# Optimization experiments

Measured on AMD Instinct MI355X. Metric: run time of the kernel, lower is better.

The kernel has to match this reference:

```python
import jax, jax.numpy as jnp
import numpy as np

EPS = 1e-8
EPS12 = 1e-12
TAU = 0.2
IOU_THRESHOLD = 0.5
NEG_INF = -1e9

N, C = 8192, 1024
HID, FGD, CLSD = 256, 64, 128


def setup_inputs() -> dict:
    key = jax.random.key(0)
    ks = jax.random.split(key, 16)
    roi_feats = jax.random.normal(ks[0], (N, C), dtype=jnp.float32)
    # labels in {-1 (ignore), 0 (bg), 1..20 (classes)}
    labels = jax.random.randint(ks[1], (N,), 0, 21, dtype=jnp.int64) - 1
    ious = jax.random.uniform(ks[2], (N,), dtype=jnp.float32)
    s = 0.02
    w1f = jax.random.normal(ks[3], (HID, C), dtype=jnp.float32) * s
    b1f = jnp.zeros((HID,), dtype=jnp.float32)
    w2f = jax.random.normal(ks[4], (FGD, HID), dtype=jnp.float32) * s
    b2f = jnp.zeros((FGD,), dtype=jnp.float32)
    w1c = jax.random.normal(ks[5], (HID, C), dtype=jnp.float32) * s
    b1c = jnp.zeros((HID,), dtype=jnp.float32)
    w2c = jax.random.normal(ks[6], (CLSD, HID), dtype=jnp.float32) * s
    b2c = jnp.zeros((CLSD,), dtype=jnp.float32)
    return {"roi_feats": roi_feats, "labels": labels, "ious": ious,
            "w1f": w1f, "b1f": b1f, "w2f": w2f, "b2f": b2f,
            "w1c": w1c, "b1c": b1c, "w2c": w2c, "b2c": b2c}


def _project_normalize(x, w1, b1, w2, b2):
    h = jax.nn.relu(x @ w1.T + b1)
    z = h @ w2.T + b2
    nrm = jnp.linalg.norm(z, axis=1, keepdims=True)  # F.normalize: z / max(||z||, eps)
    return z / jnp.maximum(nrm, EPS)


def _fg_bg_loss(z_fg, fg_mask, ignore_mask, iou_weight):
    n = z_fg.shape[0]
    anchor = fg_mask & ~ignore_mask
    eye = jnp.eye(n, dtype=bool)
    # pos_mask[i,j] = fg_mask[j] & ~ignore[j], self excluded
    pos = (fg_mask & ~ignore_mask)[None, :] & ~eye  # [N,N]
    sim = (z_fg @ z_fg.T) / TAU
    sim_exp = jnp.exp(sim) * (~eye).astype(sim.dtype)
    denom = sim_exp.sum(axis=1)  # [N]
    numer = jnp.sum(jnp.exp(sim) * pos.astype(sim.dtype), axis=1)  # [N]
    n_pos = pos.sum(axis=1)
    loss_i = -jnp.log((numer + EPS) / (denom + EPS))
    valid = anchor & (n_pos > 0)
    w = iou_weight
    num = jnp.sum(jnp.where(valid, loss_i * w, 0.0))
    den = jnp.sum(jnp.where(valid, w, 0.0)) + EPS
    return num / den


def _class_supcon_loss(z_cls, labels, fg_mask, ignore_mask, iou_weight):
    n = z_cls.shape[0]
    anchor = fg_mask & ~ignore_mask
    eye = jnp.eye(n, dtype=bool)
    valid_den = ~eye & ~ignore_mask[None, :]  # [N,N]
    # pos[i,j]: same label, j not ignored, labels[j] != 0, j != i, j valid
    pos = (labels[None, :] == labels[:, None]) & ~ignore_mask[None, :] & (labels[None, :] != 0)
    pos = pos & ~eye & valid_den
    sim = (z_cls @ z_cls.T) / TAU
    logits = jnp.where(valid_den, sim, NEG_INF)
    denom_log = jax.nn.logsumexp(logits, axis=1)  # [N]
    n_pos = pos.sum(axis=1)
    sum_pos = jnp.sum(jnp.where(pos, sim, 0.0), axis=1)
    n_pos_safe = jnp.maximum(n_pos, 1).astype(sim.dtype)
    loss_i = -(sum_pos - n_pos.astype(sim.dtype) * denom_log) / n_pos_safe
    valid = anchor & (n_pos > 0) & valid_den.any(axis=1)
    w = iou_weight
    num = jnp.sum(jnp.where(valid, loss_i * w, 0.0))
    den = jnp.sum(jnp.where(valid, w, 0.0)) + EPS12
    return num / den


def reference(roi_feats, labels, ious, w1f, b1f, w2f, b2f, w1c, b1c, w2c, b2c):
    z_fg = _project_normalize(roi_feats, w1f, b1f, w2f, b2f)
    z_cls = _project_normalize(roi_feats, w1c, b1c, w2c, b2c)
    ignore_mask = labels == -1
    bg_mask = (labels == 0) & ~ignore_mask
    fg_mask = (labels > 0) & ~ignore_mask
    iou_weight = jnp.where(ious > IOU_THRESHOLD, ious, 0.0)
    loss_fg_bg = _fg_bg_loss(z_fg, fg_mask, ignore_mask, iou_weight)
    loss_supcon = _class_supcon_loss(z_cls, labels, fg_mask, ignore_mask, iou_weight)
    # loss_weights = (1.0, 1.0); stacked as [loss_fg_bg, loss_supcon]
    return jnp.stack([loss_fg_bg * 1.0, loss_supcon * 1.0])
```

## Files before the change

### kernel.cpp

```cpp
#include <hip/hip_runtime.h>
#include <hip/hip_bf16.h>
#include <math.h>

#define N_ROI 8192
#define C_IN  1024
#define HIDD  256
#define FGD   64
#define CLSD  128
#define INV_TAU 5.0f
#define SCALE_LOG2E 7.2134752f
#define LN2F 0.69314718f

using frag_ab = __attribute__((ext_vector_type(8))) short;
using f32x16  = __attribute__((ext_vector_type(16))) float;

static __device__ __forceinline__ short f32_to_bf16_bits(float f) {
  unsigned u = __builtin_bit_cast(unsigned, f);
  u = (u + 0x7FFFu + ((u >> 16) & 1u)) >> 16;
  return (short)u;
}
static __device__ __forceinline__ float bf16_bits_to_f32(short b) {
  unsigned u = ((unsigned)(unsigned short)b) << 16;
  return __builtin_bit_cast(float, u);
}
static __device__ __forceinline__ float fast_exp2(float x) {
#if __has_builtin(__builtin_amdgcn_exp2f)
  return __builtin_amdgcn_exp2f(x);
#else
  return exp2f(x);
#endif
}

__global__ void prep_zero_kernel(float* accum, int* cnt) {
  int t = threadIdx.x;
  if (t < 8) accum[t] = 0.f;
  if (t < 24) cnt[t] = 0;
}

__global__ void prep_stats_kernel(const int* __restrict__ labels,
                                  float* __restrict__ Sfg, float* __restrict__ Pfg,
                                  float* __restrict__ Scls, float* __restrict__ SPc,
                                  float* __restrict__ pfv, float* __restrict__ nimv,
                                  float* __restrict__ ljmv, int* __restrict__ cnt) {
  int i = blockIdx.x * blockDim.x + threadIdx.x;
  if (i >= N_ROI) return;
  Sfg[i] = 0.f; Pfg[i] = 0.f; Scls[i] = 0.f; SPc[i] = 0.f;
  int l = labels[i];
  pfv[i]  = (l > 0)  ? 1.f : 0.f;
  nimv[i] = (l != -1) ? 1.f : 0.f;
  ljmv[i] = (l > 0)  ? (float)l : -7.f;
  int b = l + 1; if (b < 0) b = 0; if (b > 21) b = 21;
  atomicAdd(&cnt[b], 1);
}

__global__ __launch_bounds__(256) void pack_w_kernel(
    const float* __restrict__ w1f, const float* __restrict__ w1c,
    const float* __restrict__ w2f, const float* __restrict__ w2c,
    short* __restrict__ W1pf, short* __restrict__ W1pc,
    short* __restrict__ W2pf, short* __restrict__ W2pc) {
  int b = blockIdx.x;
  const float* src; short* dst; int Ksh; int b0;
  if (b < 128)      { src = w1f; dst = W1pf; Ksh = 10; b0 = 0; }
  else if (b < 256) { src = w1c; dst = W1pc; Ksh = 10; b0 = 128; }
  else if (b < 264) { src = w2f; dst = W2pf; Ksh = 8;  b0 = 256; }
  else              { src = w2c; dst = W2pc; Ksh = 8;  b0 = 264; }
  int K = 1 << Ksh;
  int f = (b - b0) * 256 + threadIdx.x;
  int r = f >> (Ksh - 3);
  int c0 = (f & ((K >> 3) - 1)) << 3;
  float4 v0 = *(const float4*)(src + (size_t)r * K + c0);
  float4 v1 = *(const float4*)(src + (size_t)r * K + c0 + 4);
  union { short s[8]; uint4 v; } o;
  o.s[0] = f32_to_bf16_bits(v0.x); o.s[1] = f32_to_bf16_bits(v0.y);
  o.s[2] = f32_to_bf16_bits(v0.z); o.s[3] = f32_to_bf16_bits(v0.w);
  o.s[4] = f32_to_bf16_bits(v1.x); o.s[5] = f32_to_bf16_bits(v1.y);
  o.s[6] = f32_to_bf16_bits(v1.z); o.s[7] = f32_to_bf16_bits(v1.w);
  ((uint4*)dst)[(size_t)((r >> 5) * (K >> 4) + (c0 >> 4)) * 64 +
                ((c0 >> 3) & 1) * 32 + (r & 31)] = o.v;
}

__global__ __launch_bounds__(256) void gemm1_kernel(
    const float* __restrict__ X,
    const short* __restrict__ W1pf, const short* __restrict__ W1pc,
    const float* __restrict__ b1f, const float* __restrict__ b1c,
    short* __restrict__ Hpf, short* __restrict__ Hpc) {
  __shared__ union {
    short stageA[2][1024];
    short T[4][128 * 36];
  } sm;
  int tid = threadIdx.x, lane = tid & 63, wv = tid >> 6;
  int Mb = blockIdx.x;
  const short* Wp = (wv >> 1) ? W1pc : W1pf;
  const float* b1 = (wv >> 1) ? b1c  : b1f;
  short*       Hp = (wv >> 1) ? Hpc  : Hpf;
  const uint4* Wv4 = (const uint4*)Wp;
  int arow = tid >> 3;
  int ac4  = tid & 7;
  const float* Xp = X + (size_t)(Mb * 32 + arow) * C_IN + ac4 * 4;
  int aslot = ((ac4 >> 2) * 64 + ((ac4 >> 1) & 1) * 32 + arow) * 8 + (ac4 & 1) * 4;

  float4 av;
  frag_ab breg[2][8];
  f32x16 acc[4];
  #pragma unroll
  for (int nt = 0; nt < 4; ++nt)
    #pragma unroll
    for (int q = 0; q < 16; ++q) acc[nt][q] = 0.f;

  auto loadA = [&](int c) { av = *(const float4*)(Xp + c * 32); };
  auto loadB = [&](int c, int s) {
    #pragma unroll
    for (int kci = 0; kci < 2; ++kci)
      #pragma unroll
      for (int nt = 0; nt < 4; ++nt)
        breg[s][kci * 4 + nt] =
            *(const frag_ab*)&Wv4[(size_t)(((wv & 1) * 4 + nt) * 64 + c * 2 + kci) * 64 + lane];
  };
  auto storeA = [&](int buf) {
    *(short4*)&sm.stageA[buf][aslot] =
        make_short4(f32_to_bf16_bits(av.x), f32_to_bf16_bits(av.y),
                    f32_to_bf16_bits(av.z), f32_to_bf16_bits(av.w));
  };
  auto domfma = [&](int buf, int bank) {
    frag_ab a0 = *(const frag_ab*)&sm.stageA[buf][(0 * 64 + lane) * 8];
    frag_ab a1 = *(const frag_ab*)&sm.stageA[buf][(1 * 64 + lane) * 8];
    #pragma unroll
    for (int nt = 0; nt < 4; ++nt)
      acc[nt] = __builtin_amdgcn_mfma_f32_32x32x16_bf16(a0, breg[bank][nt], acc[nt], 0, 0, 0);
    #pragma unroll
    for (int nt = 0; nt < 4; ++nt)
      acc[nt] = __builtin_amdgcn_mfma_f32_32x32x16_bf16(a1, breg[bank][4 + nt], acc[nt], 0, 0, 0);
  };

  loadA(0); loadB(0, 0); storeA(0);
  __syncthreads();
  for (int c = 0; c < 32; c += 2) {
    if (c + 1 < 32) { loadA(c + 1); loadB(c + 1, 1); }
    domfma(0, 0);
    if (c + 1 < 32) storeA(1);
    __syncthreads();
    if (c + 2 < 32) { loadA(c + 2); loadB(c + 2, 0); }
    domfma(1, 1);
    if (c + 2 < 32) storeA(0);
    __syncthreads();
  }
  int cl31 = lane & 31, h = lane >> 5;
  short* T = sm.T[wv];
  #pragma unroll
  for (int nt = 0; nt < 4; ++nt) {
    int colLocal = nt * 32 + cl31;
    float bb = b1[(wv & 1) * 128 + colLocal];
    #pragma unroll
    for (int g = 0; g < 4; ++g) {
      float x0 = fmaxf(acc[nt][g * 4 + 0] + bb, 0.f);
      float x1 = fmaxf(acc[nt][g * 4 + 1] + bb, 0.f);
      float x2 = fmaxf(acc[nt][g * 4 + 2] + bb, 0.f);
      float x3 = fmaxf(acc[nt][g * 4 + 3] + bb, 0.f);
      *(short4*)&T[colLocal * 36 + 4 * h + 8 * g] =
          make_short4(f32_to_bf16_bits(x0), f32_to_bf16_bits(x1),
                      f32_to_bf16_bits(x2), f32_to_bf16_bits(x3));
    }
  }
  __syncthreads();
  uint4* Hv4 = (uint4*)Hp;
  #pragma unroll
  for (int k = 0; k < 8; ++k) {
    union { short s[8]; uint4 v; } o;
    int c0 = k * 16 + h * 8;
    #pragma unroll
    for (int e = 0; e < 8; ++e) o.s[e] = T[(c0 + e) * 36 + cl31];
    Hv4[(size_t)(Mb * 16 + (wv & 1) * 8 + k) * 64 + h * 32 + cl31] = o.v;
  }
}

template<int D>
__device__ __forceinline__ void gemm2_head(
    const short* __restrict__ Hp, const short* __restrict__ W2p,
    const float* __restrict__ b2, short* __restrict__ Zr,
    float* __restrict__ tii, short* __restrict__ T, int gt) {
  int lane = threadIdx.x & 63;
  const frag_ab* Hv = (const frag_ab*)Hp;
  const frag_ab* Wv = (const frag_ab*)W2p;
  constexpr int NT = D / 32;
  frag_ab a[16];
  #pragma unroll
  for (int kc = 0; kc < 16; ++kc) a[kc] = Hv[(size_t)(gt * 16 + kc) * 64 + lane];
  f32x16 acc[NT];
  #pragma unroll
  for (int j = 0; j < NT; ++j)
    #pragma unroll
    for (int q = 0; q < 16; ++q) acc[j][q] = 0.f;
  #pragma unroll
  for (int kc = 0; kc < 16; ++kc)
    #pragma unroll
    for (int j = 0; j < NT; ++j)
      acc[j] = __builtin_amdgcn_mfma_f32_32x32x16_bf16(a[kc], Wv[(j * 16 + kc) * 64 + lane], acc[j], 0, 0, 0);
  int c = lane & 31, h = lane >> 5;
  float bb[NT];
  #pragma unroll
  for (int j = 0; j < NT; ++j) bb[j] = b2[j * 32 + c];
  float s1[16];
  #pragma unroll
  for (int r = 0; r < 16; ++r) {
    s1[r] = 0.f;
    #pragma unroll
    for (int j = 0; j < NT; ++j) {
      float v = acc[j][r] + bb[j];
      s1[r] += v * v;
    }
  }
  #pragma unroll
  for (int r = 0; r < 16; ++r)
    #pragma unroll
    for (int m = 1; m < 32; m <<= 1) s1[r] += __shfl_xor(s1[r], m);
  float s2[16];
  #pragma unroll
  for (int r = 0; r < 16; ++r) s2[r] = 0.f;
  #pragma unroll
  for (int j = 0; j < NT; ++j) {
    int cl = j * 32 + c;
    #pragma unroll
    for (int g = 0; g < 4; ++g) {
      short q0, q1, q2, q3;
      #pragma unroll
      for (int e = 0; e < 4; ++e) {
        int r = g * 4 + e;
        float sc = 1.f / fmaxf(sqrtf(s1[r]), 1e-8f);
        short qb = f32_to_bf16_bits((acc[j][r] + bb[j]) * sc);
        float zf = bf16_bits_to_f32(qb);
        s2[r] += zf * zf;
        if (e == 0) q0 = qb; else if (e == 1) q1 = qb; else if (e == 2) q2 = qb; else q3 = qb;
      }
      *(short4*)&T[cl * 36 + 4 * h + 8 * g] = make_short4(q0, q1, q2, q3);
    }
  }
  #pragma unroll
  for (int r = 0; r < 16; ++r)
    #pragma unroll
    for (int m = 1; m < 32; m <<= 1) s2[r] += __shfl_xor(s2[r], m);
  if (c == 0) {
    #pragma unroll
    for (int r = 0; r < 16; ++r)
      tii[gt * 32 + (r & 3) + 8 * (r >> 2) + 4 * h] = s2[r];
  }
  __syncthreads();
  uint4* Zv = (uint4*)Zr;
  #pragma unroll
  for (int k = 0; k < D / 16; ++k) {
    int c0 = (2 * k + h) * 8;
    union { short s[8]; uint4 u; } o;
    #pragma unroll
    for (int e = 0; e < 8; ++e) o.s[e] = T[(c0 + e) * 36 + c];
    Zv[(size_t)(gt * (D / 16) + k) * 64 + h * 32 + c] = o.u;
  }
}

__global__ __launch_bounds__(128) void gemm2_kernel(
    const short* __restrict__ Hpf, const short* __restrict__ Hpc,
    const short* __restrict__ W2pf, const short* __restrict__ W2pc,
    const float* __restrict__ b2f, const float* __restrict__ b2c,
    short* __restrict__ Zrf, short* __restrict__ Zrc,
    float* __restrict__ tiif, float* __restrict__ tiic) {
  __shared__ short T2[2][128 * 36];
  int wv = threadIdx.x >> 6;
  int b = blockIdx.x;
  if (b < 128)
    gemm2_head<64>(Hpf, W2pf, b2f, Zrf, tiif, T2[wv], b * 2 + wv);
  else
    gemm2_head<128>(Hpc, W2pc, b2c, Zrc, tiic, T2[wv], (b - 128) * 2 + wv);
}

template<int D, int MODE, int NJT>
__device__ __forceinline__ void loss_body(
    const short* __restrict__ Zr, const int* __restrict__ labels,
    const float* __restrict__ pfv, const float* __restrict__ nimv,
    const float* __restrict__ ljmv,
    float* __restrict__ Sg, float* __restrict__ Pg) {
  constexpr int KC = D / 16;
  int tid = threadIdx.x, lane = tid & 63, wv = tid >> 6;
  int itile = blockIdx.x * 4 + wv;
  const frag_ab* Zrv = (const frag_ab*)Zr;
  frag_ab a[KC];
  #pragma unroll
  for (int kc = 0; kc < KC; ++kc) {
    frag_ab t = Zrv[(itile * KC + kc) * 64 + lane];
    #pragma unroll
    for (int e = 0; e < 8; ++e)
      t[e] = f32_to_bf16_bits(bf16_bits_to_f32(t[e]) * SCALE_LOG2E);
    a[kc] = t;
  }
  float limf[16];
  if (MODE == 1) {
    #pragma unroll
    for (int r = 0; r < 16; ++r) {
      int row = (r & 3) + 8 * (r >> 2) + 4 * (lane >> 5);
      limf[r] = (float)labels[itile * 32 + row];
    }
  }
  float Ssum[16] = {}, Psum[16] = {};
  int jt0 = blockIdx.y * NJT;
  int jlane = lane & 31;

  #pragma unroll 2
  for (int kk = 0; kk < NJT; ++kk) {
    int jt = jt0 + kk;
    int j = jt * 32 + jlane;
    float pf = 0.f, nim = 0.f, ljm = 0.f;
    if (MODE == 0) pf = pfv[j];
    else { nim = nimv[j]; ljm = ljmv[j]; }
    f32x16 acc;
    #pragma unroll
    for (int q = 0; q < 16; ++q) acc[q] = 0.f;
    #pragma unroll
    for (int kc = 0; kc < KC; ++kc) {
      frag_ab b = Zrv[((size_t)jt * KC + kc) * 64 + lane];
      acc = __builtin_amdgcn_mfma_f32_32x32x16_bf16(a[kc], b, acc, 0, 0, 0);
    }
    #pragma unroll
    for (int rr = 0; rr < 16; ++rr) {
      float e = fast_exp2(acc[rr]);
      if (MODE == 0) {
        Ssum[rr] += e;
        Psum[rr] = fmaf(pf, e, Psum[rr]);
      } else {
        Ssum[rr] = fmaf(nim, e, Ssum[rr]);
        Psum[rr] += (limf[rr] == ljm) ? acc[rr] : 0.f;
      }
    }
  }
  #pragma unroll
  for (int r = 0; r < 16; ++r) {
    float s = Ssum[r], p = Psum[r];
    #pragma unroll
    for (int m = 1; m < 32; m <<= 1) { s += __shfl_xor(s, m); p += __shfl_xor(p, m); }
    if ((lane & 31) == 0) {
      if (MODE == 1) p *= LN2F;
      int row = (r & 3) + 8 * (r >> 2) + 4 * (lane >> 5);
      atomicAdd(&Sg[itile * 32 + row], s);
      atomicAdd(&Pg[itile * 32 + row], p);
    }
  }
}

__global__ __launch_bounds__(256, 4) void loss_kernel(
    const short* __restrict__ Zrf, const short* __restrict__ Zrc,
    const int* __restrict__ labels,
    const float* __restrict__ pfv, const float* __restrict__ nimv,
    const float* __restrict__ ljmv,
    float* __restrict__ Sfg, float* __restrict__ Pfg,
    float* __restrict__ Scls, float* __restrict__ SPc) {
  if (blockIdx.z == 0)
    loss_body<FGD, 0, 16>(Zrf, labels, pfv, nimv, ljmv, Sfg, Pfg);
  else
    loss_body<CLSD, 1, 16>(Zrc, labels, pfv, nimv, ljmv, Scls, SPc);
}

__global__ __launch_bounds__(256) void finalize_kernel(
    const float* __restrict__ Sfg, const float* __restrict__ Pfg,
    const float* __restrict__ Scls, const float* __restrict__ SPc,
    const float* __restrict__ tiif, const float* __restrict__ tiic,
    const int* __restrict__ labels, const float* __restrict__ ious,
    int* __restrict__ cnt, float* __restrict__ accum, float* __restrict__ out) {
  int i = blockIdx.x * 256 + threadIdx.x;
  int l = labels[i];
  float iv = ious[i];
  float w = (iv > 0.5f) ? iv : 0.f;
  int cntP = 0;
  #pragma unroll
  for (int b = 2; b <= 21; ++b) cntP += cnt[b];
  int cntNI = N_ROI - cnt[0];
  bool Pi = (l > 0);
  float numF = 0.f, denF = 0.f, numC = 0.f, denC = 0.f;
  float eF = __expf(INV_TAU * tiif[i]);
  float Sf = Sfg[i] - eF;
  float Pf = Pfg[i] - (Pi ? eF : 0.f);
  int nposF = cntP - (Pi ? 1 : 0);
  if (Pi && nposF > 0) {
    float lossF = logf((Sf + 1e-8f) / (Pf + 1e-8f));
    numF = lossF * w; denF = w;
  }
  float tC = INV_TAU * tiic[i];
  float eC = __expf(tC);
  float Sc = Scls[i] - ((l != -1) ? eC : 0.f);
  float SP = SPc[i] - (Pi ? tC : 0.f);
  int nposC = Pi ? (cnt[l + 1] - 1) : 0;
  bool anyv = (cntNI - ((l != -1) ? 1 : 0)) > 0;
  if (Pi && nposC > 0 && anyv) {
    float lse = logf(Sc);
    float lossC = -(SP - (float)nposC * lse) / fmaxf((float)nposC, 1.f);
    numC = lossC * w; denC = w;
  }
  float v0 = numF, v1 = denF, v2 = numC, v3 = denC;
  #pragma unroll
  for (int m = 1; m < 64; m <<= 1) {
    v0 += __shfl_xor(v0, m); v1 += __shfl_xor(v1, m);
    v2 += __shfl_xor(v2, m); v3 += __shfl_xor(v3, m);
  }
  __shared__ float red[4][4];
  int lane = threadIdx.x & 63, wid = threadIdx.x >> 6;
  if (lane == 0) { red[wid][0]=v0; red[wid][1]=v1; red[wid][2]=v2; red[wid][3]=v3; }
  __syncthreads();
  if (threadIdx.x == 0) {
    float s0=0,s1=0,s2=0,s3=0;
    for (int q = 0; q < 4; ++q) { s0+=red[q][0]; s1+=red[q][1]; s2+=red[q][2]; s3+=red[q][3]; }
    atomicAdd(&accum[0], s0); atomicAdd(&accum[1], s1);
    atomicAdd(&accum[2], s2); atomicAdd(&accum[3], s3);
    __threadfence();
    int t = atomicAdd(&cnt[22], 1);
    if (t == 31) {
      __threadfence();
      out[0] = accum[0] / (accum[1] + 1e-8f);
      out[1] = accum[2] / (accum[3] + 1e-12f);
    }
  }
}

extern "C" void kernel_launch(void* const* d_in, const int* in_sizes, int n_in,
                              void* d_out, int out_size, void* d_ws, size_t ws_size,
                              hipStream_t stream) {
  const float* X    = (const float*)d_in[0];
  const int*  labels= (const int*)d_in[1];
  const float* ious = (const float*)d_in[2];
  const float* w1f  = (const float*)d_in[3];
  const float* b1f  = (const float*)d_in[4];
  const float* w2f  = (const float*)d_in[5];
  const float* b2f  = (const float*)d_in[6];
  const float* w1c  = (const float*)d_in[7];
  const float* b1c  = (const float*)d_in[8];
  const float* w2c  = (const float*)d_in[9];
  const float* b2c  = (const float*)d_in[10];
  float* out = (float*)d_out;

  char* w = (char*)d_ws;
  short* W1pf = (short*)w;            w += 524288;
  short* W1pc = (short*)w;            w += 524288;
  short* W2pf = (short*)w;            w += 32768;
  short* W2pc = (short*)w;            w += 65536;
  short* Hpf  = (short*)w;            w += 4194304;
  short* Hpc  = (short*)w;            w += 4194304;
  short* Zrf  = (short*)w;            w += 1048576;
  short* Zrc  = (short*)w;            w += 2097152;
  float* Sfg  = (float*)w;            w += 32768;
  float* Pfg  = (float*)w;            w += 32768;
  float* Scls = (float*)w;            w += 32768;
  float* SPc  = (float*)w;            w += 32768;
  float* tiif = (float*)w;            w += 32768;
  float* tiic = (float*)w;            w += 32768;
  float* pfv  = (float*)w;            w += 32768;
  float* nimv = (float*)w;            w += 32768;
  float* ljmv = (float*)w;            w += 32768;
  float* accum= (float*)w;            w += 32;
  int*   cnt  = (int*)w;              w += 96;

  prep_zero_kernel<<<1, 64, 0, stream>>>(accum, cnt);
  prep_stats_kernel<<<N_ROI/256, 256, 0, stream>>>(labels, Sfg, Pfg, Scls, SPc,
                                                   pfv, nimv, ljmv, cnt);
  pack_w_kernel<<<280, 256, 0, stream>>>(w1f, w1c, w2f, w2c, W1pf, W1pc, W2pf, W2pc);

  gemm1_kernel<<<256, 256, 0, stream>>>(X, W1pf, W1pc, b1f, b1c, Hpf, Hpc);
  gemm2_kernel<<<256, 128, 0, stream>>>(Hpf, Hpc, W2pf, W2pc, b2f, b2c,
                                        Zrf, Zrc, tiif, tiic);

  loss_kernel<<<dim3(64, 16, 2), 256, 0, stream>>>(Zrf, Zrc, labels, pfv, nimv, ljmv,
                                                   Sfg, Pfg, Scls, SPc);

  finalize_kernel<<<N_ROI/256, 256, 0, stream>>>(Sfg, Pfg, Scls, SPc, tiif, tiic,
                                                 labels, ious, cnt, accum, out);
}
```

Baseline: 214.7 us.

## Fuse gemm1, gemm2 and label stats into one MLP kernel via LDS

Merges the first projection GEMM, the second GEMM with normalization, and the per-ROI label statistics into a single kernel. The hidden activations stay in shared memory instead of making a round trip through global memory. The accumulator zeroing moves into an extra block of the weight-packing kernel, cutting the launch count from five to two. In exchange, only two of the four waves run the second GEMM while the other two sit idle, and the kernel's larger LDS footprint may lower occupancy.

Measured after the change: 204.9 us. -4.6%, faster.

```diff
diff --git a/kernel.cpp b/kernel.cpp
--- a/kernel.cpp
+++ b/kernel.cpp
@@ -31,34 +31,19 @@
 #endif
 }
 
-__global__ void prep_zero_kernel(float* accum, int* cnt) {
-  int t = threadIdx.x;
-  if (t < 8) accum[t] = 0.f;
-  if (t < 24) cnt[t] = 0;
-}
-
-__global__ void prep_stats_kernel(const int* __restrict__ labels,
-                                  float* __restrict__ Sfg, float* __restrict__ Pfg,
-                                  float* __restrict__ Scls, float* __restrict__ SPc,
-                                  float* __restrict__ pfv, float* __restrict__ nimv,
-                                  float* __restrict__ ljmv, int* __restrict__ cnt) {
-  int i = blockIdx.x * blockDim.x + threadIdx.x;
-  if (i >= N_ROI) return;
-  Sfg[i] = 0.f; Pfg[i] = 0.f; Scls[i] = 0.f; SPc[i] = 0.f;
-  int l = labels[i];
-  pfv[i]  = (l > 0)  ? 1.f : 0.f;
-  nimv[i] = (l != -1) ? 1.f : 0.f;
-  ljmv[i] = (l > 0)  ? (float)l : -7.f;
-  int b = l + 1; if (b < 0) b = 0; if (b > 21) b = 21;
-  atomicAdd(&cnt[b], 1);
-}
-
-__global__ __launch_bounds__(256) void pack_w_kernel(
+__global__ __launch_bounds__(256) void pack_zero_kernel(
     const float* __restrict__ w1f, const float* __restrict__ w1c,
     const float* __restrict__ w2f, const float* __restrict__ w2c,
     short* __restrict__ W1pf, short* __restrict__ W1pc,
-    short* __restrict__ W2pf, short* __restrict__ W2pc) {
+    short* __restrict__ W2pf, short* __restrict__ W2pc,
+    float* __restrict__ accum, int* __restrict__ cnt) {
   int b = blockIdx.x;
+  if (b == 280) {
+    int t = threadIdx.x;
+    if (t < 8) accum[t] = 0.f;
+    if (t < 24) cnt[t] = 0;
+    return;
+  }
   const float* src; short* dst; int Ksh; int b0;
   if (b < 128)      { src = w1f; dst = W1pf; Ksh = 10; b0 = 0; }
   else if (b < 256) { src = w1c; dst = W1pc; Ksh = 10; b0 = 128; }
@@ -79,112 +64,19 @@
                 ((c0 >> 3) & 1) * 32 + (r & 31)] = o.v;
 }
 
-__global__ __launch_bounds__(256) void gemm1_kernel(
-    const float* __restrict__ X,
-    const short* __restrict__ W1pf, const short* __restrict__ W1pc,
-    const float* __restrict__ b1f, const float* __restrict__ b1c,
-    short* __restrict__ Hpf, short* __restrict__ Hpc) {
-  __shared__ union {
-    short stageA[2][1024];
-    short T[4][128 * 36];
-  } sm;
-  int tid = threadIdx.x, lane = tid & 63, wv = tid >> 6;
-  int Mb = blockIdx.x;
-  const short* Wp = (wv >> 1) ? W1pc : W1pf;
-  const float* b1 = (wv >> 1) ? b1c  : b1f;
-  short*       Hp = (wv >> 1) ? Hpc  : Hpf;
-  const uint4* Wv4 = (const uint4*)Wp;
-  int arow = tid >> 3;
-  int ac4  = tid & 7;
-  const float* Xp = X + (size_t)(Mb * 32 + arow) * C_IN + ac4 * 4;
-  int aslot = ((ac4 >> 2) * 64 + ((ac4 >> 1) & 1) * 32 + arow) * 8 + (ac4 & 1) * 4;
-
-  float4 av;
-  frag_ab breg[2][8];
-  f32x16 acc[4];
-  #pragma unroll
-  for (int nt = 0; nt < 4; ++nt)
-    #pragma unroll
-    for (int q = 0; q < 16; ++q) acc[nt][q] = 0.f;
-
-  auto loadA = [&](int c) { av = *(const float4*)(Xp + c * 32); };
-  auto loadB = [&](int c, int s) {
-    #pragma unroll
-    for (int kci = 0; kci < 2; ++kci)
-      #pragma unroll
-      for (int nt = 0; nt < 4; ++nt)
-        breg[s][kci * 4 + nt] =
-            *(const frag_ab*)&Wv4[(size_t)(((wv & 1) * 4 + nt) * 64 + c * 2 + kci) * 64 + lane];
-  };
-  auto storeA = [&](int buf) {
-    *(short4*)&sm.stageA[buf][aslot] =
-        make_short4(f32_to_bf16_bits(av.x), f32_to_bf16_bits(av.y),
-                    f32_to_bf16_bits(av.z), f32_to_bf16_bits(av.w));
-  };
-  auto domfma = [&](int buf, int bank) {
-    frag_ab a0 = *(const frag_ab*)&sm.stageA[buf][(0 * 64 + lane) * 8];
-    frag_ab a1 = *(const frag_ab*)&sm.stageA[buf][(1 * 64 + lane) * 8];
-    #pragma unroll
-    for (int nt = 0; nt < 4; ++nt)
-      acc[nt] = __builtin_amdgcn_mfma_f32_32x32x16_bf16(a0, breg[bank][nt], acc[nt], 0, 0, 0);
-    #pragma unroll
-    for (int nt = 0; nt < 4; ++nt)
-      acc[nt] = __builtin_amdgcn_mfma_f32_32x32x16_bf16(a1, breg[bank][4 + nt], acc[nt], 0, 0, 0);
-  };
-
-  loadA(0); loadB(0, 0); storeA(0);
-  __syncthreads();
-  for (int c = 0; c < 32; c += 2) {
-    if (c + 1 < 32) { loadA(c + 1); loadB(c + 1, 1); }
-    domfma(0, 0);
-    if (c + 1 < 32) storeA(1);
-    __syncthreads();
-    if (c + 2 < 32) { loadA(c + 2); loadB(c + 2, 0); }
-    domfma(1, 1);
-    if (c + 2 < 32) storeA(0);
-    __syncthreads();
-  }
-  int cl31 = lane & 31, h = lane >> 5;
-  short* T = sm.T[wv];
-  #pragma unroll
-  for (int nt = 0; nt < 4; ++nt) {
-    int colLocal = nt * 32 + cl31;
-    float bb = b1[(wv & 1) * 128 + colLocal];
-    #pragma unroll
-    for (int g = 0; g < 4; ++g) {
-      float x0 = fmaxf(acc[nt][g * 4 + 0] + bb, 0.f);
-      float x1 = fmaxf(acc[nt][g * 4 + 1] + bb, 0.f);
-      float x2 = fmaxf(acc[nt][g * 4 + 2] + bb, 0.f);
-      float x3 = fmaxf(acc[nt][g * 4 + 3] + bb, 0.f);
-      *(short4*)&T[colLocal * 36 + 4 * h + 8 * g] =
-          make_short4(f32_to_bf16_bits(x0), f32_to_bf16_bits(x1),
-                      f32_to_bf16_bits(x2), f32_to_bf16_bits(x3));
-    }
-  }
-  __syncthreads();
-  uint4* Hv4 = (uint4*)Hp;
-  #pragma unroll
-  for (int k = 0; k < 8; ++k) {
-    union { short s[8]; uint4 v; } o;
-    int c0 = k * 16 + h * 8;
-    #pragma unroll
-    for (int e = 0; e < 8; ++e) o.s[e] = T[(c0 + e) * 36 + cl31];
-    Hv4[(size_t)(Mb * 16 + (wv & 1) * 8 + k) * 64 + h * 32 + cl31] = o.v;
-  }
-}
-
 template<int D>
-__device__ __forceinline__ void gemm2_head(
-    const short* __restrict__ Hp, const short* __restrict__ W2p,
-    const float* __restrict__ b2, short* __restrict__ Zr,
-    float* __restrict__ tii, short* __restrict__ T, int gt) {
+__device__ __forceinline__ void gemm2_from_lds(
+    const short* __restrict__ T2, int coff,
+    const short* __restrict__ W2p, const float* __restrict__ b2,
+    short* __restrict__ Zr, float* __restrict__ tii,
+    short* __restrict__ T, int gt) {
   int lane = threadIdx.x & 63;
-  const frag_ab* Hv = (const frag_ab*)Hp;
   const frag_ab* Wv = (const frag_ab*)W2p;
   constexpr int NT = D / 32;
   frag_ab a[16];
   #pragma unroll
-  for (int kc = 0; kc < 16; ++kc) a[kc] = Hv[(size_t)(gt * 16 + kc) * 64 + lane];
+  for (int kc = 0; kc < 16; ++kc)
+    a[kc] = *(const frag_ab*)&T2[(lane & 31) * 516 + coff + kc * 16 + (lane >> 5) * 8];
   f32x16 acc[NT];
   #pragma unroll
   for (int j = 0; j < NT; ++j)
@@ -243,7 +135,6 @@
     for (int r = 0; r < 16; ++r)
       tii[gt * 32 + (r & 3) + 8 * (r >> 2) + 4 * h] = s2[r];
   }
-  __syncthreads();
   uint4* Zv = (uint4*)Zr;
   #pragma unroll
   for (int k = 0; k < D / 16; ++k) {
@@ -255,19 +146,111 @@
   }
 }
 
-__global__ __launch_bounds__(128) void gemm2_kernel(
-    const short* __restrict__ Hpf, const short* __restrict__ Hpc,
+__global__ __launch_bounds__(256) void fused_mlp_kernel(
+    const float* __restrict__ X,
+    const short* __restrict__ W1pf, const short* __restrict__ W1pc,
+    const float* __restrict__ b1f, const float* __restrict__ b1c,
     const short* __restrict__ W2pf, const short* __restrict__ W2pc,
     const float* __restrict__ b2f, const float* __restrict__ b2c,
     short* __restrict__ Zrf, short* __restrict__ Zrc,
-    float* __restrict__ tiif, float* __restrict__ tiic) {
-  __shared__ short T2[2][128 * 36];
-  int wv = threadIdx.x >> 6;
-  int b = blockIdx.x;
-  if (b < 128)
-    gemm2_head<64>(Hpf, W2pf, b2f, Zrf, tiif, T2[wv], b * 2 + wv);
-  else
-    gemm2_head<128>(Hpc, W2pc, b2c, Zrc, tiic, T2[wv], (b - 128) * 2 + wv);
+    float* __restrict__ tiif, float* __restrict__ tiic,
+    const int* __restrict__ labels,
+    float* __restrict__ Sfg, float* __restrict__ Pfg,
+    float* __restrict__ Scls, float* __restrict__ SPc,
+    float* __restrict__ pfv, float* __restrict__ nimv,
+    float* __restrict__ ljmv, int* __restrict__ cnt) {
+  __shared__ short stageA[2][1024];
+  __shared__ short T2[32 * 516];
+  __shared__ short Tw[2][128 * 36];
+  int tid = threadIdx.x, lane = tid & 63, wv = tid >> 6;
+  int Mb = blockIdx.x;
+
+  if (tid < 32) {
+    int i = Mb * 32 + tid;
+    Sfg[i] = 0.f; Pfg[i] = 0.f; Scls[i] = 0.f; SPc[i] = 0.f;
+    int l = labels[i];
+    pfv[i]  = (l > 0)  ? 1.f : 0.f;
+    nimv[i] = (l != -1) ? 1.f : 0.f;
+    ljmv[i] = (l > 0)  ? (float)l : -7.f;
+    int b = l + 1; if (b < 0) b = 0; if (b > 21) b = 21;
+    atomicAdd(&cnt[b], 1);
+  }
+
+  const short* Wp = (wv >> 1) ? W1pc : W1pf;
+  const float* b1 = (wv >> 1) ? b1c  : b1f;
+  const uint4* Wv4 = (const uint4*)Wp;
+  int arow = tid >> 3;
+  int ac4  = tid & 7;
+  const float* Xp = X + (size_t)(Mb * 32 + arow) * C_IN + ac4 * 4;
+  int aslot = ((ac4 >> 2) * 64 + ((ac4 >> 1) & 1) * 32 + arow) * 8 + (ac4 & 1) * 4;
+
+  float4 av;
+  frag_ab breg[2][8];
+  f32x16 acc[4];
+  #pragma unroll
+  for (int nt = 0; nt < 4; ++nt)
+    #pragma unroll
+    for (int q = 0; q < 16; ++q) acc[nt][q] = 0.f;
+
+  auto loadA = [&](int c) { av = *(const float4*)(Xp + c * 32); };
+  auto loadB = [&](int c, int s) {
+    #pragma unroll
+    for (int kci = 0; kci < 2; ++kci)
+      #pragma unroll
+      for (int nt = 0; nt < 4; ++nt)
+        breg[s][kci * 4 + nt] =
+            *(const frag_ab*)&Wv4[(size_t)(((wv & 1) * 4 + nt) * 64 + c * 2 + kci) * 64 + lane];
+  };
+  auto storeA = [&](int buf) {
+    *(short4*)&stageA[buf][aslot] =
+        make_short4(f32_to_bf16_bits(av.x), f32_to_bf16_bits(av.y),
+                    f32_to_bf16_bits(av.z), f32_to_bf16_bits(av.w));
+  };
+  auto domfma = [&](int buf, int bank) {
+    frag_ab a0 = *(const frag_ab*)&stageA[buf][(0 * 64 + lane) * 8];
+    frag_ab a1 = *(const frag_ab*)&stageA[buf][(1 * 64 + lane) * 8];
+    #pragma unroll
+    for (int nt = 0; nt < 4; ++nt)
+      acc[nt] = __builtin_amdgcn_mfma_f32_32x32x16_bf16(a0, breg[bank][nt], acc[nt], 0, 0, 0);
+    #pragma unroll
+    for (int nt = 0; nt < 4; ++nt)
+      acc[nt] = __builtin_amdgcn_mfma_f32_32x32x16_bf16(a1, breg[bank][4 + nt], acc[nt], 0, 0, 0);
+  };
+
+  loadA(0); loadB(0, 0); storeA(0);
+  __syncthreads();
+  for (int c = 0; c < 32; c += 2) {
+    if (c + 1 < 32) { loadA(c + 1); loadB(c + 1, 1); }
+    domfma(0, 0);
+    if (c + 1 < 32) storeA(1);
+    __syncthreads();
+    if (c + 2 < 32) { loadA(c + 2); loadB(c + 2, 0); }
+    domfma(1, 1);
+    if (c + 2 < 32) storeA(0);
+    __syncthreads();
+  }
+  {
+    int cl31 = lane & 31, h = lane >> 5;
+    int colHead = (wv & 1) * 128;
+    int gbase = (wv >> 1) * 256 + colHead;
+    #pragma unroll
+    for (int nt = 0; nt < 4; ++nt) {
+      float bb = b1[colHead + nt * 32 + cl31];
+      int gc = gbase + nt * 32 + cl31;
+      #pragma unroll
+      for (int q = 0; q < 16; ++q) {
+        int row = (q & 3) + 8 * (q >> 2) + 4 * h;
+        float x = fmaxf(acc[nt][q] + bb, 0.f);
+        T2[row * 516 + gc] = f32_to_bf16_bits(x);
+      }
+    }
+  }
+  __syncthreads();
+
+  if (wv == 0)
+    gemm2_from_lds<FGD>(T2, 0,   W2pf, b2f, Zrf, tiif, Tw[0], Mb);
+  else if (wv == 1)
+    gemm2_from_lds<CLSD>(T2, 256, W2pc, b2c, Zrc, tiic, Tw[1], Mb);
 }
 
 template<int D, int MODE, int NJT>
@@ -436,8 +419,6 @@
   short* W1pc = (short*)w;            w += 524288;
   short* W2pf = (short*)w;            w += 32768;
   short* W2pc = (short*)w;            w += 65536;
-  short* Hpf  = (short*)w;            w += 4194304;
-  short* Hpc  = (short*)w;            w += 4194304;
   short* Zrf  = (short*)w;            w += 1048576;
   short* Zrc  = (short*)w;            w += 2097152;
   float* Sfg  = (float*)w;            w += 32768;
@@ -452,14 +433,14 @@
   float* accum= (float*)w;            w += 32;
   int*   cnt  = (int*)w;              w += 96;
 
-  prep_zero_kernel<<<1, 64, 0, stream>>>(accum, cnt);
-  prep_stats_kernel<<<N_ROI/256, 256, 0, stream>>>(labels, Sfg, Pfg, Scls, SPc,
-                                                   pfv, nimv, ljmv, cnt);
-  pack_w_kernel<<<280, 256, 0, stream>>>(w1f, w1c, w2f, w2c, W1pf, W1pc, W2pf, W2pc);
-
-  gemm1_kernel<<<256, 256, 0, stream>>>(X, W1pf, W1pc, b1f, b1c, Hpf, Hpc);
-  gemm2_kernel<<<256, 128, 0, stream>>>(Hpf, Hpc, W2pf, W2pc, b2f, b2c,
-                                        Zrf, Zrc, tiif, tiic);
+  pack_zero_kernel<<<281, 256, 0, stream>>>(w1f, w1c, w2f, w2c,
+                                            W1pf, W1pc, W2pf, W2pc, accum, cnt);
+
+  fused_mlp_kernel<<<256, 256, 0, stream>>>(X, W1pf, W1pc, b1f, b1c,
+                                            W2pf, W2pc, b2f, b2c,
+                                            Zrf, Zrc, tiif, tiic,
+                                            labels, Sfg, Pfg, Scls, SPc,
+                                            pfv, nimv, ljmv, cnt);
 
   loss_kernel<<<dim3(64, 16, 2), 256, 0, stream>>>(Zrf, Zrc, labels, pfv, nimv, ljmv,
                                                    Sfg, Pfg, Scls, SPc);
```
